# Performance work log

Measured on AMD Instinct MI355X. Metric: run time of the kernel, lower is better.

The kernel has to match this reference:

```python
import math
import jax, jax.numpy as jnp
import numpy as np

NUM_GAUSSIANS = 1024
WIDTH = 256
HEIGHT = 256
BG_COLOR = (0.0, 0.0, 0.0)
JITTER = 1e-6


def setup_inputs() -> dict:
    key = jax.random.key(0)
    k1, k2, k3 = jax.random.split(key, 3)
    means = jax.random.normal(k1, (NUM_GAUSSIANS, 2), dtype=jnp.float32)
    # init: randn - e (keeps exp(scales) small)
    scales = jax.random.normal(k2, (NUM_GAUSSIANS, 2), dtype=jnp.float32) - math.e
    thetas = jax.random.normal(k3, (NUM_GAUSSIANS, 1), dtype=jnp.float32)
    # init: inverse_sigmoid(0.1) with eps=1e-5
    eps = 1e-5
    inv_sig = math.log((0.1 + eps) / (1.0 - 0.1 + eps))
    opacities = jnp.full((NUM_GAUSSIANS, 1), inv_sig, dtype=jnp.float32)
    return {"means": means, "scales": scales, "thetas": thetas, "opacities": opacities}


def reference(means, scales, thetas, opacities):
    # activations
    m = jnp.tanh(means)                       # [N,2] in [-1,1]
    s = jnp.exp(scales)                       # [N,2]
    th = jax.nn.sigmoid(thetas[:, 0]) * 2.0 * jnp.pi  # [N]
    op = jax.nn.sigmoid(opacities[:, 0])      # [N]

    # covariance = R diag(s^2) R^T + jitter*I, 2x2, closed form
    c, si = jnp.cos(th), jnp.sin(th)
    s2 = s * s
    a = c * c * s2[:, 0] + si * si * s2[:, 1] + JITTER   # Sigma_00
    b = c * si * (s2[:, 0] - s2[:, 1])                    # Sigma_01
    d = si * si * s2[:, 0] + c * c * s2[:, 1] + JITTER   # Sigma_11
    det = a * d - b * b
    ia, ib, id_ = d / det, -b / det, a / det              # Sigma^{-1}

    # pixel grid over [-1,1]^2
    xs = jnp.linspace(-1.0, 1.0, WIDTH, dtype=jnp.float32)
    ys = jnp.linspace(-1.0, 1.0, HEIGHT, dtype=jnp.float32)
    X, Y = jnp.meshgrid(xs, ys)               # [H,W]

    dx = X[None] - m[:, 0, None, None]        # [N,H,W]
    dy = Y[None] - m[:, 1, None, None]        # [N,H,W]
    q = (ia[:, None, None] * dx * dx
         + 2.0 * ib[:, None, None] * dx * dy
         + id_[:, None, None] * dy * dy)      # Mahalanobis dist^2
    alpha = op[:, None, None] * jnp.exp(-0.5 * q)  # [N,H,W]

    # front-to-back alpha compositing in gaussian index order
    T = jnp.cumprod(1.0 - alpha, axis=0)      # transmittance after each gaussian
    T_excl = jnp.concatenate([jnp.ones((1, HEIGHT, WIDTH), jnp.float32), T[:-1]], axis=0)
    acc = jnp.sum(alpha * T_excl, axis=0)     # [H,W], white splats

    bg = jnp.asarray(BG_COLOR, dtype=jnp.float32)
    image = acc[..., None] + T[-1][..., None] * bg   # [H,W,3]
    return image
```

## Files before the change

kernel.cpp:

```cpp
#include <hip/hip_runtime.h>
#include <math.h>

#define NG 1024
#define NWAVES 8
#define IMG_W 256
#define IMG_H 256
#define TILE 16
#define JITTER 1e-6f
#define L2E 1.4426950408889634f
#define CULL_LOG2_EPS -20.0f

__device__ __forceinline__ float fexp2(float x)  { return __builtin_amdgcn_exp2f(x); }
__device__ __forceinline__ float flog2(float x)  { return __builtin_amdgcn_logf(x); }
__device__ __forceinline__ float frcp(float x)   { return __builtin_amdgcn_rcpf(x); }
__device__ __forceinline__ float fsqrt(float x)  { return __builtin_amdgcn_sqrtf(x); }
__device__ __forceinline__ float fexp(float x)   { return fexp2(x * L2E); }
__device__ __forceinline__ float fsigmoid(float x) { return frcp(1.0f + fexp(-x)); }
__device__ __forceinline__ float ftanh(float x) {
    float t = fexp2(2.0f * L2E * x);
    return 1.0f - 2.0f * frcp(t + 1.0f);
}

__global__ __launch_bounds__(512, 2)
void gs_tiled(const float* __restrict__ means,
              const float* __restrict__ scales,
              const float* __restrict__ thetas,
              const float* __restrict__ opacities,
              float* __restrict__ out) {
    __shared__ float4 s_c0123[NG];
    __shared__ float2 s_c45[NG];
    __shared__ unsigned long long s_mask[NWAVES];
    __shared__ float2 s_seg[NWAVES][TILE * TILE];

    int tid  = threadIdx.x;
    int lane = tid & 63;
    int wave = tid >> 6;

    const float step = 2.0f / 255.0f;
    int tx = blockIdx.x & (IMG_W / TILE - 1);
    int ty = blockIdx.x >> 4;
    float rx0 = fmaf((float)(tx * TILE), step, -1.0f);
    float ry0 = fmaf((float)(ty * TILE), step, -1.0f);
    float rx1 = rx0 + (TILE - 1) * step;
    float ry1 = ry0 + (TILE - 1) * step;

    int nsurv = 0;
    #pragma unroll
    for (int k = 0; k < 2; ++k) {
        int g = k * 512 + tid;
        float mx = ftanh(means[2 * g]);
        float my = ftanh(means[2 * g + 1]);
        float s2x = fexp(2.0f * scales[2 * g]);
        float s2y = fexp(2.0f * scales[2 * g + 1]);
        float rev = fsigmoid(thetas[g]);
        float si = __builtin_amdgcn_sinf(rev);
        float c  = __builtin_amdgcn_cosf(rev);
        float a = c * c * s2x + si * si * s2y + JITTER;
        float b = c * si * (s2x - s2y);
        float d = si * si * s2x + c * c * s2y + JITTER;
        float inv_det = frcp(a * d - b * b);
        float P = -0.5f * L2E * d * inv_det;
        float Q =  L2E * b * inv_det;
        float R = -0.5f * L2E * a * inv_det;
        float l2op = flog2(fsigmoid(opacities[g]));
        float c1 = -(2.0f * P * mx + Q * my);
        float c2 = -(Q * mx + 2.0f * R * my);
        float c0 = P * mx * mx + Q * mx * my + R * my * my + l2op;

        float lam = 0.5f * ((a + d) + fsqrt((a - d) * (a - d) + 4.0f * b * b));
        float Kc = 0.5f * L2E * frcp(lam);
        float ddx = fmaxf(fmaxf(rx0 - mx, mx - rx1), 0.0f);
        float ddy = fmaxf(fmaxf(ry0 - my, my - ry1), 0.0f);
        float d2 = ddx * ddx + ddy * ddy;
        bool keep = (l2op - Kc * d2) >= CULL_LOG2_EPS;

        unsigned long long bal = __ballot(keep);
        if (lane == 0) s_mask[wave] = bal;
        __syncthreads();

        int pos = nsurv;
        #pragma unroll
        for (int w = 0; w < NWAVES; ++w) {
            unsigned long long m = s_mask[w];
            if (w < wave) pos += __popcll(m);
            nsurv += __popcll(m);
        }
        pos += __popcll(bal & ((1ull << lane) - 1ull));

        if (keep) {
            s_c0123[pos] = make_float4(c0, c1, c2, P);
            s_c45[pos]   = make_float2(Q, R);
        }
        __syncthreads();
    }

    int Ns = nsurv;
    int sbeg = __builtin_amdgcn_readfirstlane((Ns * wave) >> 3);
    int send = __builtin_amdgcn_readfirstlane((Ns * (wave + 1)) >> 3);

    int col  = lane & 15;
    int rowg = lane >> 4;
    float x  = fmaf((float)col, step, rx0);
    float y0 = fmaf((float)(rowg * 4 + 0), step, ry0);
    float y1 = y0 + step;
    float y2 = y1 + step;
    float y3 = y2 + step;

    float acc0 = 0.f, T0 = 1.f, acc1 = 0.f, T1 = 1.f;
    float acc2 = 0.f, T2 = 1.f, acc3 = 0.f, T3 = 1.f;

    #pragma unroll 4
    for (int i = sbeg; i < send; ++i) {
        float4 q = s_c0123[i];
        float2 r = s_c45[i];
        float t1 = fmaf(x, fmaf(q.w, x, q.y), q.x);
        float u  = fmaf(r.x, x, q.z);
        float e, al;
        e = fmaf(y0, fmaf(r.y, y0, u), t1); al = fexp2(e);
        acc0 = fmaf(al, T0, acc0); T0 = fmaf(-al, T0, T0);
        e = fmaf(y1, fmaf(r.y, y1, u), t1); al = fexp2(e);
        acc1 = fmaf(al, T1, acc1); T1 = fmaf(-al, T1, T1);
        e = fmaf(y2, fmaf(r.y, y2, u), t1); al = fexp2(e);
        acc2 = fmaf(al, T2, acc2); T2 = fmaf(-al, T2, T2);
        e = fmaf(y3, fmaf(r.y, y3, u), t1); al = fexp2(e);
        acc3 = fmaf(al, T3, acc3); T3 = fmaf(-al, T3, T3);
    }

    int pxb = (rowg * 4) * TILE + col;
    s_seg[wave][pxb]            = make_float2(acc0, T0);
    s_seg[wave][pxb + TILE]     = make_float2(acc1, T1);
    s_seg[wave][pxb + 2 * TILE] = make_float2(acc2, T2);
    s_seg[wave][pxb + 3 * TILE] = make_float2(acc3, T3);
    __syncthreads();

    if (tid < TILE * TILE) {
        float A = 0.0f, Tt = 1.0f;
        #pragma unroll
        for (int s = 0; s < NWAVES; ++s) {
            float2 v = s_seg[s][tid];
            A = fmaf(Tt, v.x, A);
            Tt *= v.y;
        }
        int px = tx * TILE + (tid & 15);
        int py = ty * TILE + (tid >> 4);
        float* o = out + 3 * (py * IMG_W + px);
        o[0] = A;
        o[1] = A;
        o[2] = A;
    }
}

extern "C" void kernel_launch(void* const* d_in, const int* in_sizes, int n_in,
                              void* d_out, int out_size, void* d_ws, size_t ws_size,
                              hipStream_t stream) {
    const float* means     = (const float*)d_in[0];
    const float* scales    = (const float*)d_in[1];
    const float* thetas    = (const float*)d_in[2];
    const float* opacities = (const float*)d_in[3];
    float* out = (float*)d_out;

    gs_tiled<<<dim3((IMG_W / TILE) * (IMG_H / TILE)), dim3(512), 0, stream>>>(
        means, scales, thetas, opacities, out);
}
```

Measured before the change: 65.08 us.

## Cull gaussians by exact tile-boundary maximum and loosen cull threshold

```diff
diff --git a/kernel.cpp b/kernel.cpp
--- a/kernel.cpp
+++ b/kernel.cpp
@@ -8,12 +8,11 @@
 #define TILE 16
 #define JITTER 1e-6f
 #define L2E 1.4426950408889634f
-#define CULL_LOG2_EPS -20.0f
+#define CULL_LOG2_EPS -16.0f
 
 __device__ __forceinline__ float fexp2(float x)  { return __builtin_amdgcn_exp2f(x); }
 __device__ __forceinline__ float flog2(float x)  { return __builtin_amdgcn_logf(x); }
 __device__ __forceinline__ float frcp(float x)   { return __builtin_amdgcn_rcpf(x); }
-__device__ __forceinline__ float fsqrt(float x)  { return __builtin_amdgcn_sqrtf(x); }
 __device__ __forceinline__ float fexp(float x)   { return fexp2(x * L2E); }
 __device__ __forceinline__ float fsigmoid(float x) { return frcp(1.0f + fexp(-x)); }
 __device__ __forceinline__ float ftanh(float x) {
@@ -59,20 +58,39 @@
         float b = c * si * (s2x - s2y);
         float d = si * si * s2x + c * c * s2y + JITTER;
         float inv_det = frcp(a * d - b * b);
-        float P = -0.5f * L2E * d * inv_det;
-        float Q =  L2E * b * inv_det;
-        float R = -0.5f * L2E * a * inv_det;
+        float c3 = -0.5f * L2E * d * inv_det;
+        float c4 =  L2E * b * inv_det;
+        float c5 = -0.5f * L2E * a * inv_det;
         float l2op = flog2(fsigmoid(opacities[g]));
-        float c1 = -(2.0f * P * mx + Q * my);
-        float c2 = -(Q * mx + 2.0f * R * my);
-        float c0 = P * mx * mx + Q * mx * my + R * my * my + l2op;
+        float c1 = -(2.0f * c3 * mx + c4 * my);
+        float c2 = -(c4 * mx + 2.0f * c5 * my);
+        float c0 = c3 * mx * mx + c4 * mx * my + c5 * my * my + l2op;
 
-        float lam = 0.5f * ((a + d) + fsqrt((a - d) * (a - d) + 4.0f * b * b));
-        float Kc = 0.5f * L2E * frcp(lam);
-        float ddx = fmaxf(fmaxf(rx0 - mx, mx - rx1), 0.0f);
-        float ddy = fmaxf(fmaxf(ry0 - my, my - ry1), 0.0f);
-        float d2 = ddx * ddx + ddy * ddy;
-        bool keep = (l2op - Kc * d2) >= CULL_LOG2_EPS;
+        float e2max;
+        if (mx >= rx0 && mx <= rx1 && my >= ry0 && my <= ry1) {
+            e2max = l2op;
+        } else {
+            float h3 = frcp(c3) * 0.5f;
+            float h5 = frcp(c5) * 0.5f;
+            float B0 = fmaf(c4, rx0, c2);
+            float C0 = fmaf(rx0, fmaf(c3, rx0, c1), c0);
+            float yv0 = fminf(fmaxf(-B0 * h5, ry0), ry1);
+            float v0 = fmaf(yv0, fmaf(c5, yv0, B0), C0);
+            float B1 = fmaf(c4, rx1, c2);
+            float C1 = fmaf(rx1, fmaf(c3, rx1, c1), c0);
+            float yv1 = fminf(fmaxf(-B1 * h5, ry0), ry1);
+            float v1 = fmaf(yv1, fmaf(c5, yv1, B1), C1);
+            float B2 = fmaf(c4, ry0, c1);
+            float C2 = fmaf(ry0, fmaf(c5, ry0, c2), c0);
+            float xv2 = fminf(fmaxf(-B2 * h3, rx0), rx1);
+            float v2 = fmaf(xv2, fmaf(c3, xv2, B2), C2);
+            float B3 = fmaf(c4, ry1, c1);
+            float C3 = fmaf(ry1, fmaf(c5, ry1, c2), c0);
+            float xv3 = fminf(fmaxf(-B3 * h3, rx0), rx1);
+            float v3 = fmaf(xv3, fmaf(c3, xv3, B3), C3);
+            e2max = fmaxf(fmaxf(v0, v1), fmaxf(v2, v3));
+        }
+        bool keep = e2max >= CULL_LOG2_EPS;
 
         unsigned long long bal = __ballot(keep);
         if (lane == 0) s_mask[wave] = bal;
@@ -88,8 +106,8 @@
         pos += __popcll(bal & ((1ull << lane) - 1ull));
 
         if (keep) {
-            s_c0123[pos] = make_float4(c0, c1, c2, P);
-            s_c45[pos]   = make_float2(Q, R);
+            s_c0123[pos] = make_float4(c0, c1, c2, c3);
+            s_c45[pos]   = make_float2(c4, c5);
         }
         __syncthreads();
     }
```

Result: faster. 63.32 us (-2.7%).
